# Performance work log

Measured on AMD Instinct MI355X. Metric: run time of the kernel, lower is better.

## Reference

```python
import jax, jax.numpy as jnp
import numpy as np

S, B, D, H, V = 1024, 4, 1024, 4096, 32000
EPS = 1e-5

def _ln(x, g, b):
    m = jnp.mean(x, axis=-1, keepdims=True)
    v = jnp.var(x, axis=-1, keepdims=True)
    return (x - m) * jax.lax.rsqrt(v + EPS) * g + b

def setup_inputs() -> dict:
    key = jax.random.key(0)
    ks = jax.random.split(key, 12)
    def xav(k, shape):
        fan_in, fan_out = shape[1], shape[0]
        lim = np.sqrt(6.0 / (fan_in + fan_out))
        return jax.random.uniform(k, shape, jnp.float32, -lim, lim)
    return {
        "inputs": jax.random.randint(ks[0], (S, B), 0, V, dtype=jnp.int32),
        "emb_table": jax.random.normal(ks[1], (V, D), jnp.float32),
        "WQ": xav(ks[2], (D, D)),
        "WK": xav(ks[3], (D, D)),
        "WV": xav(ks[4], (D, D)),
        "Wo": xav(ks[5], (D, D)),
        "bo": jnp.zeros((D,), jnp.float32),
        "W1": xav(ks[6], (H, D)),
        "b1": jnp.zeros((H,), jnp.float32),
        "W2": xav(ks[7], (D, H)),
        "b2": jnp.zeros((D,), jnp.float32),
        "g1": jnp.ones((D,), jnp.float32),
        "be1": jnp.zeros((D,), jnp.float32),
        "g2": jnp.ones((D,), jnp.float32),
        "be2": jnp.zeros((D,), jnp.float32),
        "Wd": xav(ks[8], (V, D)),
        "bd": jnp.zeros((V,), jnp.float32),
    }

def reference(inputs, emb_table, WQ, WK, WV, Wo, bo, W1, b1, W2, b2, g1, be1, g2, be2, Wd, bd):
    # inputs: [S, B] int ids
    emb = emb_table[inputs]                       # [S, B, D]
    # F.linear(x, W) == x @ W.T
    Q = jnp.einsum('sbd,ed->bse', emb, WQ)        # [B, S, D]
    K = jnp.einsum('sbd,ed->bse', emb, WK)
    Vv = jnp.einsum('sbd,ed->bse', emb, WV)
    scores = jnp.einsum('bqd,bkd->bqk', Q, K) / jnp.sqrt(jnp.float32(D))
    attn = jax.nn.softmax(scores, axis=-1)        # [B, S, S]
    z = jnp.einsum('bqk,bkd->qbd', attn, Vv)      # back to [S, B, D]
    z = jnp.einsum('sbd,ed->sbe', z, Wo) + bo
    x = _ln(emb + z, g1, be1)
    ffn = jnp.einsum('sbh,dh->sbd', jax.nn.relu(jnp.einsum('sbd,hd->sbh', x, W1) + b1), W2) + b2
    out = _ln(x + ffn, g2, be2)
    logits = out.reshape(S * B, D) @ Wd.T + bd    # [S*B, V]
    return logits
```

## Files before the change

kernel.cpp:

```cpp
#include <hip/hip_runtime.h>

typedef float f32x4 __attribute__((ext_vector_type(4)));
typedef __bf16 bf16x8 __attribute__((ext_vector_type(8)));
typedef int i32x4 __attribute__((ext_vector_type(4)));
typedef unsigned short u16;
typedef unsigned short u16x4 __attribute__((ext_vector_type(4)));
typedef unsigned short u16x8 __attribute__((ext_vector_type(8)));
typedef unsigned int u32;

#define SEQ 1024
#define NBATCH 4
#define DM 1024
#define HD 4096
#define NV 32000
#define NT (SEQ * NBATCH)

__device__ __forceinline__ u16 f2bf(float f) {
  u32 u = __builtin_bit_cast(u32, f);
  return (u16)((u + 0x7FFFu + ((u >> 16) & 1u)) >> 16);
}

__global__ __launch_bounds__(256) void cast_all_kernel(
    const float* __restrict__ wq, const float* __restrict__ wk,
    const float* __restrict__ wv, const float* __restrict__ wo,
    const float* __restrict__ w1, const float* __restrict__ w2,
    u16* __restrict__ wqk, u16* __restrict__ wvh, u16* __restrict__ woh,
    u16* __restrict__ w1h, u16* __restrict__ w2h) {
  long i = (long)blockIdx.x * 256 + threadIdx.x;
  const float* src;
  u16* dst;
  long off;
  if (i < 262144) {
    if (i < 131072) { src = wq; off = i; } else { src = wk; off = i - 131072; }
    dst = wqk + i * 8;
  } else if (i < 393216) {
    src = wv; off = i - 262144; dst = wvh + off * 8;
  } else if (i < 524288) {
    src = wo; off = i - 393216; dst = woh + off * 8;
  } else if (i < 1048576) {
    src = w1; off = i - 524288; dst = w1h + off * 8;
  } else {
    src = w2; off = i - 1048576; dst = w2h + off * 8;
  }
  const f32x4* p = (const f32x4*)(src + off * 8);
  f32x4 a = p[0], b = p[1];
  u16x8 o;
  o[0] = f2bf(a[0]); o[1] = f2bf(a[1]); o[2] = f2bf(a[2]); o[3] = f2bf(a[3]);
  o[4] = f2bf(b[0]); o[5] = f2bf(b[1]); o[6] = f2bf(b[2]); o[7] = f2bf(b[3]);
  *(u16x8*)dst = o;
}

__global__ __launch_bounds__(256) void embed_kernel(const int* __restrict__ ids,
                                                    const float* __restrict__ tab,
                                                    float* __restrict__ ef,
                                                    u16* __restrict__ eh) {
  int t = blockIdx.x, tid = threadIdx.x;
  long id = ids[t];
  f32x4 v = *(const f32x4*)(tab + id * DM + tid * 4);
  *(f32x4*)(ef + (long)t * DM + tid * 4) = v;
  u16x4 h;
  h[0] = f2bf(v[0]); h[1] = f2bf(v[1]); h[2] = f2bf(v[2]); h[3] = f2bf(v[3]);
  *(u16x4*)(eh + (long)t * DM + tid * 4) = h;
}

__global__ __launch_bounds__(256) void softmax_kernel(const float* __restrict__ s,
                                                      u16* __restrict__ p) {
  int row = blockIdx.x, tid = threadIdx.x;
  const float* rp = s + (long)row * SEQ;
  f32x4 v = *(const f32x4*)(rp + tid * 4);
  float mx = fmaxf(fmaxf(v[0], v[1]), fmaxf(v[2], v[3]));
  for (int o = 32; o; o >>= 1) mx = fmaxf(mx, __shfl_xor(mx, o));
  __shared__ float red[4];
  if ((tid & 63) == 0) red[tid >> 6] = mx;
  __syncthreads();
  mx = fmaxf(fmaxf(red[0], red[1]), fmaxf(red[2], red[3]));
  const float sc = 0.03125f;
  f32x4 e;
  e[0] = expf((v[0] - mx) * sc); e[1] = expf((v[1] - mx) * sc);
  e[2] = expf((v[2] - mx) * sc); e[3] = expf((v[3] - mx) * sc);
  float sm = e[0] + e[1] + e[2] + e[3];
  for (int o = 32; o; o >>= 1) sm += __shfl_xor(sm, o);
  __syncthreads();
  if ((tid & 63) == 0) red[tid >> 6] = sm;
  __syncthreads();
  sm = red[0] + red[1] + red[2] + red[3];
  float inv = 1.0f / sm;
  u16x4 o4;
  o4[0] = f2bf(e[0] * inv); o4[1] = f2bf(e[1] * inv);
  o4[2] = f2bf(e[2] * inv); o4[3] = f2bf(e[3] * inv);
  *(u16x4*)(p + (long)row * SEQ + tid * 4) = o4;
}

__global__ __launch_bounds__(256) void ln_kernel(const float* __restrict__ in,
                                                 const float* __restrict__ g,
                                                 const float* __restrict__ be,
                                                 float* __restrict__ outf,
                                                 u16* __restrict__ outh) {
  int row = blockIdx.x, tid = threadIdx.x;
  f32x4 v = *(const f32x4*)(in + (long)row * DM + tid * 4);
  float s = v[0] + v[1] + v[2] + v[3];
  float q = v[0] * v[0] + v[1] * v[1] + v[2] * v[2] + v[3] * v[3];
  for (int o = 32; o; o >>= 1) { s += __shfl_xor(s, o); q += __shfl_xor(q, o); }
  __shared__ float rs_[4], rq_[4];
  if ((tid & 63) == 0) { rs_[tid >> 6] = s; rq_[tid >> 6] = q; }
  __syncthreads();
  s = rs_[0] + rs_[1] + rs_[2] + rs_[3];
  q = rq_[0] + rq_[1] + rq_[2] + rq_[3];
  float mean = s * (1.0f / DM);
  float var = q * (1.0f / DM) - mean * mean;
  float rstd = rsqrtf(var + 1e-5f);
  f32x4 gg = *(const f32x4*)(g + tid * 4);
  f32x4 bb = *(const f32x4*)(be + tid * 4);
  f32x4 y;
  y[0] = (v[0] - mean) * rstd * gg[0] + bb[0];
  y[1] = (v[1] - mean) * rstd * gg[1] + bb[1];
  y[2] = (v[2] - mean) * rstd * gg[2] + bb[2];
  y[3] = (v[3] - mean) * rstd * gg[3] + bb[3];
  if (outf) *(f32x4*)(outf + (long)row * DM + tid * 4) = y;
  if (outh) {
    u16x4 h;
    h[0] = f2bf(y[0]); h[1] = f2bf(y[1]); h[2] = f2bf(y[2]); h[3] = f2bf(y[3]);
    *(u16x4*)(outh + (long)row * DM + tid * 4) = h;
  }
}

__global__ __launch_bounds__(256) void ln_i8_kernel(const float* __restrict__ in,
                                                    const float* __restrict__ g,
                                                    const float* __restrict__ be,
                                                    char* __restrict__ q8,
                                                    float* __restrict__ scale) {
  int row = blockIdx.x, tid = threadIdx.x;
  f32x4 v = *(const f32x4*)(in + (long)row * DM + tid * 4);
  float s = v[0] + v[1] + v[2] + v[3];
  float q = v[0] * v[0] + v[1] * v[1] + v[2] * v[2] + v[3] * v[3];
  for (int o = 32; o; o >>= 1) { s += __shfl_xor(s, o); q += __shfl_xor(q, o); }
  __shared__ float rs_[4], rq_[4], rm_[4];
  if ((tid & 63) == 0) { rs_[tid >> 6] = s; rq_[tid >> 6] = q; }
  __syncthreads();
  s = rs_[0] + rs_[1] + rs_[2] + rs_[3];
  q = rq_[0] + rq_[1] + rq_[2] + rq_[3];
  float mean = s * (1.0f / DM);
  float var = q * (1.0f / DM) - mean * mean;
  float rstd = rsqrtf(var + 1e-5f);
  f32x4 gg = *(const f32x4*)(g + tid * 4);
  f32x4 bb = *(const f32x4*)(be + tid * 4);
  f32x4 y;
  y[0] = (v[0] - mean) * rstd * gg[0] + bb[0];
  y[1] = (v[1] - mean) * rstd * gg[1] + bb[1];
  y[2] = (v[2] - mean) * rstd * gg[2] + bb[2];
  y[3] = (v[3] - mean) * rstd * gg[3] + bb[3];
  float am = fmaxf(fmaxf(fabsf(y[0]), fabsf(y[1])), fmaxf(fabsf(y[2]), fabsf(y[3])));
  for (int o = 32; o; o >>= 1) am = fmaxf(am, __shfl_xor(am, o));
  __syncthreads();
  if ((tid & 63) == 0) rm_[tid >> 6] = am;
  __syncthreads();
  am = fmaxf(fmaxf(rm_[0], rm_[1]), fmaxf(rm_[2], rm_[3]));
  float inv = (am > 0.f) ? 127.f / am : 0.f;
  int q0 = (int)rintf(y[0] * inv), q1 = (int)rintf(y[1] * inv);
  int q2 = (int)rintf(y[2] * inv), q3 = (int)rintf(y[3] * inv);
  u32 pk = (q0 & 255) | ((q1 & 255) << 8) | ((q2 & 255) << 16) | ((u32)(q3 & 255) << 24);
  *(u32*)(q8 + (size_t)row * DM + tid * 4) = pk;
  if (tid == 0) scale[row] = am * (1.0f / 127.f);
}

__global__ __launch_bounds__(256) void rowq_i8_kernel(const float* __restrict__ in,
                                                      char* __restrict__ q8,
                                                      float* __restrict__ scale) {
  int row = blockIdx.x, tid = threadIdx.x;
  f32x4 v = *(const f32x4*)(in + (size_t)row * DM + tid * 4);
  float am = fmaxf(fmaxf(fabsf(v[0]), fabsf(v[1])), fmaxf(fabsf(v[2]), fabsf(v[3])));
  for (int o = 32; o; o >>= 1) am = fmaxf(am, __shfl_xor(am, o));
  __shared__ float rm_[4];
  if ((tid & 63) == 0) rm_[tid >> 6] = am;
  __syncthreads();
  am = fmaxf(fmaxf(rm_[0], rm_[1]), fmaxf(rm_[2], rm_[3]));
  float inv = (am > 0.f) ? 127.f / am : 0.f;
  int q0 = (int)rintf(v[0] * inv), q1 = (int)rintf(v[1] * inv);
  int q2 = (int)rintf(v[2] * inv), q3 = (int)rintf(v[3] * inv);
  u32 pk = (q0 & 255) | ((q1 & 255) << 8) | ((q2 & 255) << 16) | ((u32)(q3 & 255) << 24);
  *(u32*)(q8 + (size_t)row * DM + tid * 4) = pk;
  if (tid == 0) scale[row] = am * (1.0f / 127.f);
}

#define GLD(gp, lp)                                              \
  __builtin_amdgcn_global_load_lds(                              \
      (__attribute__((address_space(1))) void*)(gp),             \
      (__attribute__((address_space(3))) void*)(lp), 16, 0, 0)

#define BM 128
#define BN 128
#define BK 32

__global__ __launch_bounds__(256) void gemm_bt(
    const u16* __restrict__ A, const u16* __restrict__ B,
    float* __restrict__ Cf, u16* __restrict__ Ch,
    const float* __restrict__ bias, const float* __restrict__ resid,
    int K, int lda, int ldb, int ldc,
    long batA, long batB, long batC, int relu) {
  __shared__ u16 As[BM * BK];
  __shared__ u16 Bs[BN * BK];
  const int tid = threadIdx.x;
  const int bz = blockIdx.z;
  A += (long)bz * batA;
  B += (long)bz * batB;
  const long cbase = (long)bz * batC;
  const int row0 = blockIdx.y * BM;
  const int col0 = blockIdx.x * BN;
  const int l = tid & 63;
  const int w = tid >> 6;
  const int wr = (w >> 1) * 64, wc = (w & 1) * 64;

  f32x4 acc[4][4] = {};

  const u16* gA = A + (long)(row0 + (tid >> 2)) * lda + (tid & 3) * 8;
  const u16* gB = B + (long)(col0 + (tid >> 2)) * ldb + (tid & 3) * 8;
  const long a64 = (long)64 * lda, b64 = (long)64 * ldb;
  u16* lA = As + tid * 8;
  u16* lB = Bs + tid * 8;

  const int fr = l & 15;
  const int fk = (l >> 4) * 8;
  const u16* rA = As + (wr + fr) * BK + fk;
  const u16* rB = Bs + (wc + fr) * BK + fk;

  for (int k0 = 0; k0 < K; k0 += BK) {
    GLD(gA + k0, lA);
    GLD(gA + a64 + k0, lA + 2048);
    GLD(gB + k0, lB);
    GLD(gB + b64 + k0, lB + 2048);
    __syncthreads();
    bf16x8 af[4], bf[4];
#pragma unroll
    for (int m = 0; m < 4; ++m) af[m] = *(const bf16x8*)(rA + m * 16 * BK);
#pragma unroll
    for (int n = 0; n < 4; ++n) bf[n] = *(const bf16x8*)(rB + n * 16 * BK);
#pragma unroll
    for (int m = 0; m < 4; ++m)
#pragma unroll
      for (int n = 0; n < 4; ++n)
        acc[m][n] = __builtin_amdgcn_mfma_f32_16x16x32_bf16(af[m], bf[n], acc[m][n], 0, 0, 0);
    __syncthreads();
  }

  const int er = row0 + wr + ((l >> 4) << 2);
  const int ec = col0 + wc + (l & 15);
#pragma unroll
  for (int m = 0; m < 4; ++m) {
#pragma unroll
    for (int n = 0; n < 4; ++n) {
      f32x4 v = acc[m][n];
      const int c = ec + n * 16;
      float bv = bias ? bias[c] : 0.0f;
#pragma unroll
      for (int i = 0; i < 4; ++i) {
        const int r = er + m * 16 + i;
        float x = v[i] + bv;
        if (resid) x += resid[(long)r * ldc + c];
        if (relu) x = fmaxf(x, 0.0f);
        if (Cf) Cf[cbase + (long)r * ldc + c] = x;
        if (Ch) Ch[cbase + (long)r * ldc + c] = f2bf(x);
      }
    }
  }
}

#define DSB() __builtin_amdgcn_sched_barrier(0)
#define SBAR() __builtin_amdgcn_s_barrier()

__global__ __launch_bounds__(256) void gemm_i8(
    const char* __restrict__ A, const char* __restrict__ B,
    float* __restrict__ C, const float* __restrict__ sA, const float* __restrict__ sB,
    const float* __restrict__ bias, int K, int lda, int ldb, int ldc,
    int Mtiles, int Ntiles) {
  __shared__ __align__(16) char As[3][128 * 64];
  __shared__ __align__(16) char Bs[3][128 * 64];
  const int tid = threadIdx.x;

  const int nwg = gridDim.x;
  const int blk = blockIdx.x;
  const int cpx = nwg >> 3;
  const int wg = (blk & 7) * cpx + (blk >> 3);
  const int row0 = (wg / Ntiles) * 128;
  const int col0 = (wg % Ntiles) * 128;

  const int l = tid & 63;
  const int w = tid >> 6;
  const int wr = (w >> 1) * 64, wc = (w & 1) * 64;

  const int srow = tid >> 2;
  const int sslot = (tid & 3) ^ ((srow >> 1) & 3);
  const char* gA = A + (size_t)(row0 + srow) * lda + sslot * 16;
  const char* gB = B + (size_t)(col0 + srow) * ldb + sslot * 16;
  const size_t a64 = (size_t)64 * lda, b64 = (size_t)64 * ldb;

#define STAGE_I8(buf, kt)                                            \
  do {                                                               \
    const char* _ga = gA + (size_t)(kt) * 64;                        \
    const char* _gb = gB + (size_t)(kt) * 64;                        \
    GLD(_ga, &As[buf][0] + tid * 16);                                \
    GLD(_ga + a64, &As[buf][4096] + tid * 16);                       \
    GLD(_gb, &Bs[buf][0] + tid * 16);                                \
    GLD(_gb + b64, &Bs[buf][4096] + tid * 16);                       \
  } while (0)

  const int fr = l & 15;
  const int fsw = 16 * ((l >> 4) ^ ((fr >> 1) & 3));
  const int raoff = (wr + fr) * 64 + fsw;
  const int rboff = (wc + fr) * 64 + fsw;

  i32x4 acc[4][4] = {};

#define COMPUTE_I8(buf)                                                         \
  do {                                                                          \
    i32x4 af[4], bf[4];                                                         \
    _Pragma("unroll")                                                           \
    for (int m = 0; m < 4; ++m) af[m] = *(const i32x4*)(&As[buf][raoff + m * 1024]); \
    _Pragma("unroll")                                                           \
    for (int n = 0; n < 4; ++n) bf[n] = *(const i32x4*)(&Bs[buf][rboff + n * 1024]); \
    _Pragma("unroll")                                                           \
    for (int m = 0; m < 4; ++m)                                                 \
      _Pragma("unroll")                                                         \
      for (int n = 0; n < 4; ++n)                                               \
        acc[m][n] = __builtin_amdgcn_mfma_i32_16x16x64_i8(af[m], bf[n], acc[m][n], 0, 0, 0); \
  } while (0)

#define PIPE_STEP(bufS, kt, bufC)                    \
  do {                                               \
    STAGE_I8(bufS, kt);                              \
    COMPUTE_I8(bufC);                                \
    asm volatile("s_waitcnt vmcnt(4)"); DSB();       \
    SBAR();                                          \
  } while (0)

  const int nkt = K >> 6;

  STAGE_I8(0, 0);
  STAGE_I8(1, 1);
  asm volatile("s_waitcnt vmcnt(4)"); DSB();
  SBAR();

  for (int t = 0; t + 7 <= nkt; t += 3) {
    PIPE_STEP(2, t + 2, 0);
    PIPE_STEP(0, t + 3, 1);
    PIPE_STEP(1, t + 4, 2);
  }
  PIPE_STEP(2, 14, 0);
  PIPE_STEP(0, 15, 1);
  COMPUTE_I8(2);
  asm volatile("s_waitcnt vmcnt(0)"); DSB();
  SBAR();
  COMPUTE_I8(0);

  const int er = row0 + wr + ((l >> 4) << 2);
  const int ec = col0 + wc + (l & 15);
#pragma unroll
  for (int m = 0; m < 4; ++m) {
#pragma unroll
    for (int n = 0; n < 4; ++n) {
      i32x4 v = acc[m][n];
      const int c = ec + n * 16;
      const float sb = sB[c];
      const float bv = bias ? bias[c] : 0.0f;
#pragma unroll
      for (int i = 0; i < 4; ++i) {
        const int r = er + m * 16 + i;
        C[(size_t)r * ldc + c] = (float)v[i] * (sA[r] * sb) + bv;
      }
    }
  }
#undef STAGE_I8
#undef COMPUTE_I8
#undef PIPE_STEP
}

template <int N0, int N1>
__device__ __forceinline__ void mfma16(f32x4 (&acc)[8][4], const bf16x8 (&af)[8],
                                       bf16x8 b0, bf16x8 b1) {
#pragma unroll
  for (int m = 0; m < 8; ++m) {
    acc[m][N0] = __builtin_amdgcn_mfma_f32_16x16x32_bf16(af[m], b0, acc[m][N0], 0, 0, 0);
    acc[m][N1] = __builtin_amdgcn_mfma_f32_16x16x32_bf16(af[m], b1, acc[m][N1], 0, 0, 0);
  }
}

__global__ __launch_bounds__(512, 2) void gemm256_bt(
    const u16* __restrict__ A, const u16* __restrict__ B,
    float* __restrict__ Cf, u16* __restrict__ Ch,
    const float* __restrict__ bias,
    int K, int lda, int ldb, int ldc, int Mtiles, int Ntiles, int relu) {
  __shared__ __align__(16) u16 As[2][2][128 * 64];
  __shared__ __align__(16) u16 Bs[2][2][256 * 32];
  const int tid = threadIdx.x;

  const int nwg = gridDim.x;
  const int blk = blockIdx.x;
  const int cpx = nwg >> 3;
  const int wg = (blk & 7) * cpx + (blk >> 3);
  const int gsz = 4 * Ntiles;
  const int gid = wg / gsz;
  const int rem = wg - gid * gsz;
  const int row0 = (gid * 4 + (rem & 3)) * 256;
  const int col0 = (rem >> 2) * 256;

  const int l = tid & 63;
  const int w = tid >> 6;
  const int wr = w >> 2;
  const int wc = w & 3;

  const int sArow = tid >> 3;
  const int sAcol = ((tid & 7) ^ ((sArow >> 1) & 7)) * 8;
  const int sBrow = tid >> 2;
  const int sBcol = ((tid & 3) ^ ((sBrow >> 2) & 3)) * 8;

  const u16* gA = A + (size_t)(row0 + sArow) * lda + sAcol;
  const u16* gB = B + (size_t)(col0 + sBrow) * ldb + sBcol;
  const size_t a64 = (size_t)64 * lda;
  const size_t b128 = (size_t)128 * ldb;

#define STAGE_A(buf, h, kt)                                          \
  do {                                                               \
    const u16* _g = gA + (size_t)(h) * 128 * lda + (size_t)(kt) * 64;\
    u16* _l = &As[buf][h][0] + tid * 8;                              \
    GLD(_g, _l);                                                     \
    GLD(_g + a64, _l + 4096);                                        \
  } while (0)
#define STAGE_B(buf, kk, kt)                                         \
  do {                                                               \
    const u16* _g = gB + (size_t)(kt) * 64 + (kk) * 32;              \
    u16* _l = &Bs[buf][kk][0] + tid * 8;                             \
    GLD(_g, _l);                                                     \
    GLD(_g + b128, _l + 4096);                                       \
  } while (0)

  const int fr = l & 15;
  const int g8 = (l >> 4) * 8;
  const int acp0 = g8 ^ (((fr >> 1) & 7) * 8);
  const int acp1 = (32 + g8) ^ (((fr >> 1) & 7) * 8);
  const int bcp = g8 ^ (((fr >> 2) & 3) * 8);

#define RA(buf, m, cp) (*(const bf16x8*)(&As[buf][wr][((m) * 16 + fr) * 64 + (cp)]))
#define RB(buf, n, kk) (*(const bf16x8*)(&Bs[buf][kk][(wc * 64 + (n) * 16 + fr) * 32 + bcp]))

  f32x4 acc[8][4] = {};
  bf16x8 a0[8], a1[8], bb0, bb1;

  const int nkt = K >> 6;
  const int nit = nkt >> 1;

  STAGE_A(0, 0, 0); STAGE_A(0, 1, 0);
  STAGE_B(0, 0, 0); STAGE_B(0, 1, 0);
  STAGE_B(1, 0, 1); STAGE_A(1, 0, 1);
  asm volatile("s_waitcnt vmcnt(4)"); DSB();
  SBAR();

  for (int i = 0; i < nit; ++i) {
    const int u = 2 * i + 1;
    const int v = (2 * i + 2 < nkt) ? 2 * i + 2 : nkt - 1;
    const int w2 = (2 * i + 3 < nkt) ? 2 * i + 3 : nkt - 1;

#pragma unroll
    for (int m = 0; m < 8; ++m) a0[m] = RA(0, m, acp0);
    bb0 = RB(0, 0, 0); bb1 = RB(0, 1, 0);
    STAGE_A(1, 1, u);
    SBAR();
    asm volatile("s_waitcnt lgkmcnt(0)"); DSB();
    __builtin_amdgcn_s_setprio(1);
    mfma16<0, 1>(acc, a0, bb0, bb1);
    __builtin_amdgcn_s_setprio(0);
    SBAR();
    bb0 = RB(0, 2, 0); bb1 = RB(0, 3, 0);
    STAGE_B(1, 1, u);
    asm volatile("s_waitcnt vmcnt(6)"); DSB();
    SBAR();
    asm volatile("s_waitcnt lgkmcnt(0)"); DSB();
    __builtin_amdgcn_s_setprio(1);
    mfma16<2, 3>(acc, a0, bb0, bb1);
    __builtin_amdgcn_s_setprio(0);
    SBAR();
#pragma unroll
    for (int m = 0; m < 8; ++m) a1[m] = RA(0, m, acp1);
    bb0 = RB(0, 0, 1); bb1 = RB(0, 1, 1);
    STAGE_B(0, 0, v);
    SBAR();
    asm volatile("s_waitcnt lgkmcnt(0)"); DSB();
    __builtin_amdgcn_s_setprio(1);
    mfma16<0, 1>(acc, a1, bb0, bb1);
    __builtin_amdgcn_s_setprio(0);
    SBAR();
    bb0 = RB(0, 2, 1); bb1 = RB(0, 3, 1);
    STAGE_A(0, 0, v);
    asm volatile("s_waitcnt vmcnt(6)"); DSB();
    SBAR();
    asm volatile("s_waitcnt lgkmcnt(0)"); DSB();
    __builtin_amdgcn_s_setprio(1);
    mfma16<2, 3>(acc, a1, bb0, bb1);
    __builtin_amdgcn_s_setprio(0);
    SBAR();
#pragma unroll
    for (int m = 0; m < 8; ++m) a0[m] = RA(1, m, acp0);
    bb0 = RB(1, 0, 0); bb1 = RB(1, 1, 0);
    STAGE_A(0, 1, v);
    SBAR();
    asm volatile("s_waitcnt lgkmcnt(0)"); DSB();
    __builtin_amdgcn_s_setprio(1);
    mfma16<0, 1>(acc, a0, bb0, bb1);
    __builtin_amdgcn_s_setprio(0);
    SBAR();
    bb0 = RB(1, 2, 0); bb1 = RB(1, 3, 0);
    STAGE_B(0, 1, v);
    asm volatile("s_waitcnt vmcnt(6)"); DSB();
    SBAR();
    asm volatile("s_waitcnt lgkmcnt(0)"); DSB();
    __builtin_amdgcn_s_setprio(1);
    mfma16<2, 3>(acc, a0, bb0, bb1);
    __builtin_amdgcn_s_setprio(0);
    SBAR();
#pragma unroll
    for (int m = 0; m < 8; ++m) a1[m] = RA(1, m, acp1);
    bb0 = RB(1, 0, 1); bb1 = RB(1, 1, 1);
    STAGE_B(1, 0, w2);
    SBAR();
    asm volatile("s_waitcnt lgkmcnt(0)"); DSB();
    __builtin_amdgcn_s_setprio(1);
    mfma16<0, 1>(acc, a1, bb0, bb1);
    __builtin_amdgcn_s_setprio(0);
    SBAR();
    bb0 = RB(1, 2, 1); bb1 = RB(1, 3, 1);
    STAGE_A(1, 0, w2);
    asm volatile("s_waitcnt vmcnt(6)"); DSB();
    SBAR();
    asm volatile("s_waitcnt lgkmcnt(0)"); DSB();
    __builtin_amdgcn_s_setprio(1);
    mfma16<2, 3>(acc, a1, bb0, bb1);
    __builtin_amdgcn_s_setprio(0);
    SBAR();
  }

  asm volatile("s_waitcnt vmcnt(0)"); DSB();

  const int er = row0 + wr * 128 + ((l >> 4) << 2);
  const int ec = col0 + wc * 64 + (l & 15);
#pragma unroll
  for (int m = 0; m < 8; ++m) {
#pragma unroll
    for (int n = 0; n < 4; ++n) {
      f32x4 vv = acc[m][n];
      const int c = ec + n * 16;
      float bv = bias ? bias[c] : 0.0f;
#pragma unroll
      for (int i = 0; i < 4; ++i) {
        const int r = er + m * 16 + i;
        float x = vv[i] + bv;
        if (relu) x = fmaxf(x, 0.0f);
        if (Cf) Cf[(size_t)r * ldc + c] = x;
        if (Ch) Ch[(size_t)r * ldc + c] = f2bf(x);
      }
    }
  }
#undef STAGE_A
#undef STAGE_B
#undef RA
#undef RB
}

extern "C" void kernel_launch(void* const* d_in, const int* in_sizes, int n_in,
                              void* d_out, int out_size, void* d_ws, size_t ws_size,
                              hipStream_t stream) {
  const int* ids = (const int*)d_in[0];
  const float* tab = (const float*)d_in[1];
  const float* WQ = (const float*)d_in[2];
  const float* WK = (const float*)d_in[3];
  const float* WV = (const float*)d_in[4];
  const float* Wo = (const float*)d_in[5];
  const float* bo = (const float*)d_in[6];
  const float* W1 = (const float*)d_in[7];
  const float* b1 = (const float*)d_in[8];
  const float* W2 = (const float*)d_in[9];
  const float* b2 = (const float*)d_in[10];
  const float* g1 = (const float*)d_in[11];
  const float* be1 = (const float*)d_in[12];
  const float* g2 = (const float*)d_in[13];
  const float* be2 = (const float*)d_in[14];
  const float* Wd = (const float*)d_in[15];
  const float* bd = (const float*)d_in[16];
  float* logits = (float*)d_out;

  if (ws_size < 280000000ull) return;

  char* p = (char*)d_ws;
  auto alloc = [&](size_t bytes) {
    char* r = p;
    p += (bytes + 255) & ~(size_t)255;
    return r;
  };
  float* embf = (float*)alloc((size_t)NT * DM * 4);
  u16* embh = (u16*)alloc((size_t)NT * DM * 2);
  u16* WQKh = (u16*)alloc((size_t)2 * DM * DM * 2);
  u16* WVh = (u16*)alloc((size_t)DM * DM * 2);
  u16* Woh = (u16*)alloc((size_t)DM * DM * 2);
  u16* W1h = (u16*)alloc((size_t)HD * DM * 2);
  u16* W2h = (u16*)alloc((size_t)DM * HD * 2);
  char* Wdq = (char*)alloc((size_t)NV * DM);
  float* sWd = (float*)alloc((size_t)NV * 4);
  u16* QKh = (u16*)alloc((size_t)NT * 2 * DM * 2);
  u16* VTh = (u16*)alloc((size_t)NBATCH * DM * SEQ * 2);
  float* scoresf = (float*)alloc((size_t)NBATCH * SEQ * SEQ * 4);
  u16* Ph = (u16*)alloc((size_t)NBATCH * SEQ * SEQ * 2);
  u16* zh = (u16*)alloc((size_t)NT * DM * 2);
  float* r1f = (float*)alloc((size_t)NT * DM * 4);
  float* xf = (float*)alloc((size_t)NT * DM * 4);
  u16* xh = (u16*)alloc((size_t)NT * DM * 2);
  u16* hh = (u16*)alloc((size_t)NT * HD * 2);
  float* r2f = (float*)alloc((size_t)NT * DM * 4);
  char* outq = (char*)alloc((size_t)NT * DM);
  float* sOut = (float*)alloc((size_t)NT * 4);

  cast_all_kernel<<<dim3(6144), 256, 0, stream>>>(WQ, WK, WV, Wo, W1, W2,
                                                  WQKh, WVh, Woh, W1h, W2h);
  rowq_i8_kernel<<<dim3(NV), 256, 0, stream>>>(Wd, Wdq, sWd);

  embed_kernel<<<NT, 256, 0, stream>>>(ids, tab, embf, embh);

  gemm_bt<<<dim3(2 * DM / BN, NT / BM, 1), 256, 0, stream>>>(
      embh, WQKh, nullptr, QKh, nullptr, nullptr, DM, DM, DM, 2 * DM, 0, 0, 0, 0);

  gemm_bt<<<dim3(SEQ / BN, DM / BM, NBATCH), 256, 0, stream>>>(
      WVh, embh, nullptr, VTh, nullptr, nullptr, DM, DM, NBATCH * DM, SEQ,
      0, DM, (long)DM * SEQ, 0);

  gemm_bt<<<dim3(SEQ / BN, SEQ / BM, NBATCH), 256, 0, stream>>>(
      QKh, QKh + DM, scoresf, nullptr, nullptr, nullptr, DM,
      NBATCH * 2 * DM, NBATCH * 2 * DM, SEQ,
      2 * DM, 2 * DM, (long)SEQ * SEQ, 0);

  softmax_kernel<<<NBATCH * SEQ, 256, 0, stream>>>(scoresf, Ph);

  gemm_bt<<<dim3(DM / BN, SEQ / BM, NBATCH), 256, 0, stream>>>(
      Ph, VTh, nullptr, zh, nullptr, nullptr, SEQ, SEQ, SEQ, NBATCH * DM,
      (long)SEQ * SEQ, (long)DM * SEQ, DM, 0);

  gemm_bt<<<dim3(DM / BN, NT / BM, 1), 256, 0, stream>>>(
      zh, Woh, r1f, nullptr, bo, embf, DM, DM, DM, DM, 0, 0, 0, 0);

  ln_kernel<<<NT, 256, 0, stream>>>(r1f, g1, be1, xf, xh);

  gemm256_bt<<<dim3((NT / 256) * (HD / 256)), 512, 0, stream>>>(
      xh, W1h, nullptr, hh, b1, DM, DM, DM, HD, NT / 256, HD / 256, 1);
  gemm_bt<<<dim3(DM / BN, NT / BM, 1), 256, 0, stream>>>(
      hh, W2h, r2f, nullptr, b2, xf, HD, HD, HD, DM, 0, 0, 0, 0);

  ln_i8_kernel<<<NT, 256, 0, stream>>>(r2f, g2, be2, outq, sOut);

  gemm_i8<<<dim3((NT / 128) * (NV / 128)), 256, 0, stream>>>(
      outq, Wdq, logits, sOut, sWd, bd, DM, DM, DM, NV, NT / 128, NV / 128);
}
```

Before: 712.1 us.

## Run FFN down-projection as int8 GEMM with per-row quantized activations and W2

Measured after the change: 656.7 us. 1.08x faster.

```diff
diff --git a/kernel.cpp b/kernel.cpp
--- a/kernel.cpp
+++ b/kernel.cpp
@@ -19,13 +19,16 @@
   u32 u = __builtin_bit_cast(u32, f);
   return (u16)((u + 0x7FFFu + ((u >> 16) & 1u)) >> 16);
 }
+__device__ __forceinline__ float bf2f(u16 h) {
+  return __builtin_bit_cast(float, (u32)h << 16);
+}
 
 __global__ __launch_bounds__(256) void cast_all_kernel(
     const float* __restrict__ wq, const float* __restrict__ wk,
     const float* __restrict__ wv, const float* __restrict__ wo,
-    const float* __restrict__ w1, const float* __restrict__ w2,
+    const float* __restrict__ w1,
     u16* __restrict__ wqk, u16* __restrict__ wvh, u16* __restrict__ woh,
-    u16* __restrict__ w1h, u16* __restrict__ w2h) {
+    u16* __restrict__ w1h) {
   long i = (long)blockIdx.x * 256 + threadIdx.x;
   const float* src;
   u16* dst;
@@ -37,10 +40,8 @@
     src = wv; off = i - 262144; dst = wvh + off * 8;
   } else if (i < 524288) {
     src = wo; off = i - 393216; dst = woh + off * 8;
-  } else if (i < 1048576) {
+  } else {
     src = w1; off = i - 524288; dst = w1h + off * 8;
-  } else {
-    src = w2; off = i - 1048576; dst = w2h + off * 8;
   }
   const f32x4* p = (const f32x4*)(src + off * 8);
   f32x4 a = p[0], b = p[1];
@@ -163,22 +164,73 @@
   if (tid == 0) scale[row] = am * (1.0f / 127.f);
 }
 
-__global__ __launch_bounds__(256) void rowq_i8_kernel(const float* __restrict__ in,
-                                                      char* __restrict__ q8,
-                                                      float* __restrict__ scale) {
-  int row = blockIdx.x, tid = threadIdx.x;
-  f32x4 v = *(const f32x4*)(in + (size_t)row * DM + tid * 4);
-  float am = fmaxf(fmaxf(fabsf(v[0]), fabsf(v[1])), fmaxf(fabsf(v[2]), fabsf(v[3])));
+__global__ __launch_bounds__(256) void rowq_f32(const float* __restrict__ in,
+                                                char* __restrict__ q8,
+                                                float* __restrict__ scale, int rowlen) {
+  const int row = blockIdx.x, tid = threadIdx.x;
+  const float* rp = in + (size_t)row * rowlen;
+  const int nch = rowlen >> 10;
+  f32x4 v0 = {}, v1 = {}, v2 = {}, v3 = {};
+  v0 = *(const f32x4*)(rp + tid * 4);
+  if (nch > 1) v1 = *(const f32x4*)(rp + 1024 + tid * 4);
+  if (nch > 2) v2 = *(const f32x4*)(rp + 2048 + tid * 4);
+  if (nch > 3) v3 = *(const f32x4*)(rp + 3072 + tid * 4);
+  auto am4 = [](f32x4 v) {
+    return fmaxf(fmaxf(fabsf(v[0]), fabsf(v[1])), fmaxf(fabsf(v[2]), fabsf(v[3])));
+  };
+  float am = fmaxf(fmaxf(am4(v0), am4(v1)), fmaxf(am4(v2), am4(v3)));
   for (int o = 32; o; o >>= 1) am = fmaxf(am, __shfl_xor(am, o));
   __shared__ float rm_[4];
   if ((tid & 63) == 0) rm_[tid >> 6] = am;
   __syncthreads();
   am = fmaxf(fmaxf(rm_[0], rm_[1]), fmaxf(rm_[2], rm_[3]));
-  float inv = (am > 0.f) ? 127.f / am : 0.f;
-  int q0 = (int)rintf(v[0] * inv), q1 = (int)rintf(v[1] * inv);
-  int q2 = (int)rintf(v[2] * inv), q3 = (int)rintf(v[3] * inv);
-  u32 pk = (q0 & 255) | ((q1 & 255) << 8) | ((q2 & 255) << 16) | ((u32)(q3 & 255) << 24);
-  *(u32*)(q8 + (size_t)row * DM + tid * 4) = pk;
+  const float inv = (am > 0.f) ? 127.f / am : 0.f;
+  auto pack = [&](f32x4 v) {
+    int q0 = (int)rintf(v[0] * inv), q1 = (int)rintf(v[1] * inv);
+    int q2 = (int)rintf(v[2] * inv), q3 = (int)rintf(v[3] * inv);
+    return (u32)((q0 & 255) | ((q1 & 255) << 8) | ((q2 & 255) << 16) | ((u32)(q3 & 255) << 24));
+  };
+  char* qp = q8 + (size_t)row * rowlen;
+  *(u32*)(qp + tid * 4) = pack(v0);
+  if (nch > 1) *(u32*)(qp + 1024 + tid * 4) = pack(v1);
+  if (nch > 2) *(u32*)(qp + 2048 + tid * 4) = pack(v2);
+  if (nch > 3) *(u32*)(qp + 3072 + tid * 4) = pack(v3);
+  if (tid == 0) scale[row] = am * (1.0f / 127.f);
+}
+
+__global__ __launch_bounds__(256) void rowq_bf16_hd(const u16* __restrict__ in,
+                                                    char* __restrict__ q8,
+                                                    float* __restrict__ scale) {
+  const int row = blockIdx.x, tid = threadIdx.x;
+  const u16* rp = in + (size_t)row * HD;
+  f32x4 v0, v1, v2, v3;
+  auto ld4 = [&](int off) {
+    u16x4 h = *(const u16x4*)(rp + off + tid * 4);
+    f32x4 v;
+    v[0] = bf2f(h[0]); v[1] = bf2f(h[1]); v[2] = bf2f(h[2]); v[3] = bf2f(h[3]);
+    return v;
+  };
+  v0 = ld4(0); v1 = ld4(1024); v2 = ld4(2048); v3 = ld4(3072);
+  auto am4 = [](f32x4 v) {
+    return fmaxf(fmaxf(fabsf(v[0]), fabsf(v[1])), fmaxf(fabsf(v[2]), fabsf(v[3])));
+  };
+  float am = fmaxf(fmaxf(am4(v0), am4(v1)), fmaxf(am4(v2), am4(v3)));
+  for (int o = 32; o; o >>= 1) am = fmaxf(am, __shfl_xor(am, o));
+  __shared__ float rm_[4];
+  if ((tid & 63) == 0) rm_[tid >> 6] = am;
+  __syncthreads();
+  am = fmaxf(fmaxf(rm_[0], rm_[1]), fmaxf(rm_[2], rm_[3]));
+  const float inv = (am > 0.f) ? 127.f / am : 0.f;
+  auto pack = [&](f32x4 v) {
+    int q0 = (int)rintf(v[0] * inv), q1 = (int)rintf(v[1] * inv);
+    int q2 = (int)rintf(v[2] * inv), q3 = (int)rintf(v[3] * inv);
+    return (u32)((q0 & 255) | ((q1 & 255) << 8) | ((q2 & 255) << 16) | ((u32)(q3 & 255) << 24));
+  };
+  char* qp = q8 + (size_t)row * HD;
+  *(u32*)(qp + tid * 4) = pack(v0);
+  *(u32*)(qp + 1024 + tid * 4) = pack(v1);
+  *(u32*)(qp + 2048 + tid * 4) = pack(v2);
+  *(u32*)(qp + 3072 + tid * 4) = pack(v3);
   if (tid == 0) scale[row] = am * (1.0f / 127.f);
 }
 
@@ -270,8 +322,8 @@
 __global__ __launch_bounds__(256) void gemm_i8(
     const char* __restrict__ A, const char* __restrict__ B,
     float* __restrict__ C, const float* __restrict__ sA, const float* __restrict__ sB,
-    const float* __restrict__ bias, int K, int lda, int ldb, int ldc,
-    int Mtiles, int Ntiles) {
+    const float* __restrict__ bias, const float* __restrict__ resid,
+    int K, int lda, int ldb, int ldc, int Mtiles, int Ntiles) {
   __shared__ __align__(16) char As[3][128 * 64];
   __shared__ __align__(16) char Bs[3][128 * 64];
   const int tid = threadIdx.x;
@@ -344,8 +396,8 @@
     PIPE_STEP(0, t + 3, 1);
     PIPE_STEP(1, t + 4, 2);
   }
-  PIPE_STEP(2, 14, 0);
-  PIPE_STEP(0, 15, 1);
+  PIPE_STEP(2, nkt - 2, 0);
+  PIPE_STEP(0, nkt - 1, 1);
   COMPUTE_I8(2);
   asm volatile("s_waitcnt vmcnt(0)"); DSB();
   SBAR();
@@ -364,7 +416,9 @@
 #pragma unroll
       for (int i = 0; i < 4; ++i) {
         const int r = er + m * 16 + i;
-        C[(size_t)r * ldc + c] = (float)v[i] * (sA[r] * sb) + bv;
+        float x = (float)v[i] * (sA[r] * sb) + bv;
+        if (resid) x += resid[(size_t)r * ldc + c];
+        C[(size_t)r * ldc + c] = x;
       }
     }
   }
@@ -599,7 +653,8 @@
   u16* WVh = (u16*)alloc((size_t)DM * DM * 2);
   u16* Woh = (u16*)alloc((size_t)DM * DM * 2);
   u16* W1h = (u16*)alloc((size_t)HD * DM * 2);
-  u16* W2h = (u16*)alloc((size_t)DM * HD * 2);
+  char* W2q = (char*)alloc((size_t)DM * HD);
+  float* sW2 = (float*)alloc((size_t)DM * 4);
   char* Wdq = (char*)alloc((size_t)NV * DM);
   float* sWd = (float*)alloc((size_t)NV * 4);
   u16* QKh = (u16*)alloc((size_t)NT * 2 * DM * 2);
@@ -611,13 +666,16 @@
   float* xf = (float*)alloc((size_t)NT * DM * 4);
   u16* xh = (u16*)alloc((size_t)NT * DM * 2);
   u16* hh = (u16*)alloc((size_t)NT * HD * 2);
+  char* hq = (char*)alloc((size_t)NT * HD);
+  float* sH = (float*)alloc((size_t)NT * 4);
   float* r2f = (float*)alloc((size_t)NT * DM * 4);
   char* outq = (char*)alloc((size_t)NT * DM);
   float* sOut = (float*)alloc((size_t)NT * 4);
 
-  cast_all_kernel<<<dim3(6144), 256, 0, stream>>>(WQ, WK, WV, Wo, W1, W2,
-                                                  WQKh, WVh, Woh, W1h, W2h);
-  rowq_i8_kernel<<<dim3(NV), 256, 0, stream>>>(Wd, Wdq, sWd);
+  cast_all_kernel<<<dim3(4096), 256, 0, stream>>>(WQ, WK, WV, Wo, W1,
+                                                  WQKh, WVh, Woh, W1h);
+  rowq_f32<<<dim3(NV), 256, 0, stream>>>(Wd, Wdq, sWd, DM);
+  rowq_f32<<<dim3(DM), 256, 0, stream>>>(W2, W2q, sW2, HD);
 
   embed_kernel<<<NT, 256, 0, stream>>>(ids, tab, embf, embh);
 
@@ -646,11 +704,14 @@
 
   gemm256_bt<<<dim3((NT / 256) * (HD / 256)), 512, 0, stream>>>(
       xh, W1h, nullptr, hh, b1, DM, DM, DM, HD, NT / 256, HD / 256, 1);
-  gemm_bt<<<dim3(DM / BN, NT / BM, 1), 256, 0, stream>>>(
-      hh, W2h, r2f, nullptr, b2, xf, HD, HD, HD, DM, 0, 0, 0, 0);
+
+  rowq_bf16_hd<<<dim3(NT), 256, 0, stream>>>(hh, hq, sH);
+
+  gemm_i8<<<dim3((NT / 128) * (DM / 128)), 256, 0, stream>>>(
+      hq, W2q, r2f, sH, sW2, b2, xf, HD, HD, HD, DM, NT / 128, DM / 128);
 
   ln_i8_kernel<<<NT, 256, 0, stream>>>(r2f, g2, be2, outq, sOut);
 
   gemm_i8<<<dim3((NT / 128) * (NV / 128)), 256, 0, stream>>>(
-      outq, Wdq, logits, sOut, sWd, bd, DM, DM, DM, NV, NT / 128, NV / 128);
-}
+      outq, Wdq, logits, sOut, sWd, bd, nullptr, DM, DM, DM, NV, NT / 128, NV / 128);
+}
```
